# Performance work log

Hardware: AMD Instinct MI355X
Metric: run time of the kernel (lower is better)

The kernel has to match this reference:

```python
import jax, jax.numpy as jnp
import numpy as np

EMBED_DIM = 768
NUM_HEADS = 12
HEAD_DIM = EMBED_DIM // NUM_HEADS


def setup_inputs() -> dict:
    key = jax.random.key(0)
    k1, k2, k3, k4, k5 = jax.random.split(key, 5)
    B, S, D = 2, 4096, EMBED_DIM
    scale = 1.0 / np.sqrt(D)
    return {
        "x": jax.random.normal(k1, (B, S, D), dtype=jnp.float32),
        "Wqkv": jax.random.normal(k2, (D, 3 * D), dtype=jnp.float32) * scale,
        "bqkv": jax.random.normal(k3, (3 * D,), dtype=jnp.float32) * 0.02,
        "Wout": jax.random.normal(k4, (D, D), dtype=jnp.float32) * scale,
        "bout": jax.random.normal(k5, (D,), dtype=jnp.float32) * 0.02,
    }


def reference(x, Wqkv, bqkv, Wout, bout):
    B, S, D = x.shape
    H, Hd = NUM_HEADS, HEAD_DIM
    # fused QKV projection: [B,S,3D]
    qkv = x @ Wqkv + bqkv
    q, k, v = jnp.split(qkv, 3, axis=-1)
    # [B,S,D] -> [B,H,S,Hd]
    q = q.reshape(B, S, H, Hd).transpose(0, 2, 1, 3)
    k = k.reshape(B, S, H, Hd).transpose(0, 2, 1, 3)
    v = v.reshape(B, S, H, Hd).transpose(0, 2, 1, 3)
    # causal SDPA (dropout_p = 0)
    scores = jnp.einsum("bhsd,bhtd->bhst", q, k) / jnp.sqrt(jnp.asarray(Hd, x.dtype))
    causal = jnp.tril(jnp.ones((S, S), dtype=bool))  # [S,S]
    scores = jnp.where(causal[None, None], scores, jnp.finfo(x.dtype).min)
    attn = jax.nn.softmax(scores, axis=-1)
    y = jnp.einsum("bhst,bhtd->bhsd", attn, v)  # [B,H,S,Hd]
    y = y.transpose(0, 2, 1, 3).reshape(B, S, D)
    return y @ Wout + bout
```

## Files before the change

### kernel.cpp

```cpp
#include <hip/hip_runtime.h>

#define S_LEN 4096
#define NH 12
#define HD 64
#define DMODEL 768
#define BATCH 2
#define MTOT (BATCH * S_LEN)

typedef __bf16 bf16x8 __attribute__((ext_vector_type(8)));
typedef __bf16 bf16x4 __attribute__((ext_vector_type(4)));
typedef float f32x4 __attribute__((ext_vector_type(4)));
typedef float f32x8 __attribute__((ext_vector_type(8)));

#define SM_SCALE_LOG2E 0.18033688f
#define SLAB_STRIDE 8448

__device__ __forceinline__ f32x4 f32x4_zero() {
  f32x4 z = {0.f, 0.f, 0.f, 0.f};
  return z;
}

__device__ __forceinline__ void async16(const __bf16* g, void* l) {
  __builtin_amdgcn_global_load_lds(
      (const __attribute__((address_space(1))) void*)g,
      (__attribute__((address_space(3))) void*)l, 16, 0, 0);
}

__global__ __launch_bounds__(256) void cvt_f32_bf16(const float* __restrict__ in,
                                                    __bf16* __restrict__ out, int n8) {
  int i = blockIdx.x * 256 + threadIdx.x;
  if (i >= n8) return;
  f32x8 a = ((const f32x8*)in)[i];
  bf16x8 o;
#pragma unroll
  for (int j = 0; j < 8; ++j) o[j] = (__bf16)a[j];
  ((bf16x8*)out)[i] = o;
}

__global__ __launch_bounds__(256) void transpose_cvt(const float* __restrict__ in,
                                                     __bf16* __restrict__ out, int N) {
  __shared__ __bf16 t[64][72];
  int kb = blockIdx.x * 64, nb = blockIdx.y * 64;
  int c = threadIdx.x & 63, r0 = threadIdx.x >> 6;
#pragma unroll
  for (int i = 0; i < 16; ++i) {
    int r = r0 * 16 + i;
    t[c][r] = (__bf16)in[(size_t)(kb + r) * N + nb + c];
  }
  __syncthreads();
#pragma unroll
  for (int i = 0; i < 16; ++i) {
    int r = r0 * 16 + i;
    out[(size_t)(nb + r) * DMODEL + kb + c] = t[r][c];
  }
}

__device__ __forceinline__ void gemm128_bt(const __bf16* __restrict__ A,
                                           const __bf16* __restrict__ Bt,
                                           int m0, int n0, int K,
                                           __bf16* Alds, __bf16* Blds,
                                           f32x4 acc[4][4]) {
  const int tid = threadIdx.x;
  const int l = tid & 63, w = tid >> 6;
  const int wr = w >> 1, wc = w & 1;
  const int g = l >> 4, ln = l & 15;

  const int rr = tid >> 3;
  const int sx = (tid & 7) ^ (rr & 7);
  const __bf16* As = A + (size_t)(m0 + rr) * K + sx * 8;
  const __bf16* Bs = Bt + (size_t)(n0 + rr) * K + sx * 8;
  char* Ad = (char*)Alds + (w << 10);
  char* Bd = (char*)Blds + (w << 10);

  for (int k0 = 0; k0 < K; k0 += 64) {
#pragma unroll
    for (int i = 0; i < 4; ++i) {
      async16(As + (size_t)(i * 32) * K + k0, Ad + i * 4096);
      async16(Bs + (size_t)(i * 32) * K + k0, Bd + i * 4096);
    }
    __syncthreads();
#pragma unroll
    for (int kk = 0; kk < 2; ++kk) {
      bf16x8 af[4], bfr[4];
#pragma unroll
      for (int mi = 0; mi < 4; ++mi) {
        int row = wr * 64 + mi * 16 + ln;
        af[mi] = *(const bf16x8*)(Alds + row * 64 + ((((kk << 2) + g) ^ (row & 7)) << 3));
      }
#pragma unroll
      for (int ni = 0; ni < 4; ++ni) {
        int row = wc * 64 + ni * 16 + ln;
        bfr[ni] = *(const bf16x8*)(Blds + row * 64 + ((((kk << 2) + g) ^ (row & 7)) << 3));
      }
#pragma unroll
      for (int mi = 0; mi < 4; ++mi)
#pragma unroll
        for (int ni = 0; ni < 4; ++ni)
          acc[mi][ni] =
              __builtin_amdgcn_mfma_f32_16x16x32_bf16(af[mi], bfr[ni], acc[mi][ni], 0, 0, 0);
    }
    __syncthreads();
  }
}

__global__ __launch_bounds__(256) void gemm_qkv(const __bf16* __restrict__ xb,
                                                const __bf16* __restrict__ Wt,
                                                const float* __restrict__ bqkv,
                                                __bf16* __restrict__ Qo,
                                                __bf16* __restrict__ Ko,
                                                __bf16* __restrict__ Vto) {
  __shared__ __bf16 Alds[128 * 64];
  __shared__ __bf16 Blds[128 * 64];
  int bm = blockIdx.x & 63, bn = blockIdx.x >> 6;
  int m0 = bm * 128, n0 = bn * 128;
  f32x4 acc[4][4];
#pragma unroll
  for (int i = 0; i < 4; ++i)
#pragma unroll
    for (int j = 0; j < 4; ++j) acc[i][j] = f32x4_zero();
  gemm128_bt(xb, Wt, m0, n0, DMODEL, Alds, Blds, acc);

  const int l = threadIdx.x & 63, w = threadIdx.x >> 6;
  const int wr = w >> 1, wc = w & 1, g = l >> 4, ln = l & 15;
#pragma unroll
  for (int ni = 0; ni < 4; ++ni) {
    int ncol = n0 + wc * 64 + ni * 16 + ln;
    int which = ncol / DMODEL;
    int dd = ncol - which * DMODEL;
    int h = dd >> 6, hd = dd & 63;
    float bias = bqkv[ncol];
    if (which == 2) {
#pragma unroll
      for (int mi = 0; mi < 4; ++mi)
#pragma unroll
        for (int r = 0; r < 4; ++r) {
          int mrow = m0 + wr * 64 + mi * 16 + 4 * g + r;
          int b = mrow >> 12, s = mrow & (S_LEN - 1);
          float v = acc[mi][ni][r] + bias;
          Vto[(((size_t)(b * NH + h) * HD) + hd) * S_LEN + s] = (__bf16)v;
        }
    } else {
      __bf16* op = (which == 0) ? Qo : Ko;
      const float scl = (which == 0) ? SM_SCALE_LOG2E : 1.0f;
#pragma unroll
      for (int mi = 0; mi < 4; ++mi)
#pragma unroll
        for (int r = 0; r < 4; ++r) {
          int mrow = m0 + wr * 64 + mi * 16 + 4 * g + r;
          int b = mrow >> 12, s = mrow & (S_LEN - 1);
          float v = (acc[mi][ni][r] + bias) * scl;
          op[((((size_t)b * NH + h) * S_LEN) + s) * HD + hd] = (__bf16)v;
        }
    }
  }
}

__global__ __launch_bounds__(256) void gemm_out(const __bf16* __restrict__ yb,
                                                const __bf16* __restrict__ Wt,
                                                const float* __restrict__ bout,
                                                float* __restrict__ out) {
  __shared__ __bf16 Alds[128 * 64];
  __shared__ __bf16 Blds[128 * 64];
  int bm = blockIdx.x & 63, bn = blockIdx.x >> 6;
  int m0 = bm * 128, n0 = bn * 128;
  f32x4 acc[4][4];
#pragma unroll
  for (int i = 0; i < 4; ++i)
#pragma unroll
    for (int j = 0; j < 4; ++j) acc[i][j] = f32x4_zero();
  gemm128_bt(yb, Wt, m0, n0, DMODEL, Alds, Blds, acc);

  const int l = threadIdx.x & 63, w = threadIdx.x >> 6;
  const int wr = w >> 1, wc = w & 1, g = l >> 4, ln = l & 15;
#pragma unroll
  for (int ni = 0; ni < 4; ++ni) {
    int ncol = n0 + wc * 64 + ni * 16 + ln;
    float bias = bout[ncol];
#pragma unroll
    for (int mi = 0; mi < 4; ++mi)
#pragma unroll
      for (int r = 0; r < 4; ++r) {
        int mrow = m0 + wr * 64 + mi * 16 + 4 * g + r;
        out[(size_t)mrow * DMODEL + ncol] = acc[mi][ni][r] + bias;
      }
  }
}

__global__ __launch_bounds__(256) void attn_fwd17(const __bf16* __restrict__ Q,
                                                  const __bf16* __restrict__ K,
                                                  const __bf16* __restrict__ Vt,
                                                  __bf16* __restrict__ Y,
                                                  char* __restrict__ Po) {
  __shared__ __bf16 KVl[2][2][4096];
  __shared__ char Plb[4][2048];

  const int tid = threadIdx.x;
  const int wv = tid >> 6, l = tid & 63;
  const int g = l >> 4, ln = l & 15;
  const int bi = blockIdx.x;
  const int xcd = bi & 7, j = bi >> 3;
  const int head = xcd * 3 + (j % 3);
  const int r_ = j / 3;

  int c, part, np;
  bool split;
  if (r_ < 64) {
    c = 63 - (r_ >> 2);
    part = r_ & 3;
    np = 4;
    split = true;
  } else if (r_ < 112) {
    int q = r_ - 64;
    c = 47 - q / 3;
    part = q % 3;
    np = 3;
    split = true;
  } else if (r_ < 144) {
    int q = r_ - 112;
    c = 31 - (q >> 1);
    part = q & 1;
    np = 2;
    split = true;
  } else {
    c = 159 - r_;
    part = 0;
    np = 1;
    split = false;
  }
  const int T = c + 1;
  const int base = T / np, rem = T % np;
  const int t0 = part * base + (part < rem ? part : rem);
  const int t1 = t0 + base + (part < rem ? 1 : 0);

  const int q0 = 64 * c + 16 * wv;
  const int thr = 16 * wv + ln;
  const bool hasDiag = (t1 == T);

  const size_t hb = (size_t)head * (S_LEN * HD);
  const __bf16* Qh = Q + hb;
  const __bf16* Kh = K + hb;
  const __bf16* Vh = Vt + hb;

  const int sw = (ln & 7) << 4;
  char* Pw = Plb[wv] + ln * 128;

  const int r0 = tid >> 3;
  const int s0 = (tid & 7) ^ (r0 & 7);
  const size_t kL0 = (size_t)r0 * HD + s0 * 8;
  const size_t kL1 = kL0 + (size_t)32 * HD;
  const size_t vL0 = (size_t)r0 * S_LEN + s0 * 8;
  const size_t vL1 = vL0 + (size_t)32 * S_LEN;
  const int ldsoff = wv << 10;

  bf16x8 qf[2];
#pragma unroll
  for (int t = 0; t < 2; ++t)
    qf[t] = *(const bf16x8*)(Qh + (size_t)(q0 + ln) * HD + 32 * t + 8 * g);

  bf16x8 ones;
#pragma unroll
  for (int t = 0; t < 8; ++t) ones[t] = (__bf16)1.0f;

  f32x4 o[4], o5;
#pragma unroll
  for (int nt = 0; nt < 4; ++nt) o[nt] = f32x4_zero();
  o5 = f32x4_zero();

  const __bf16* kq = Kh + (size_t)t0 * 64 * HD;
  const __bf16* vq = Vh + t0 * 64;
  {
    char* Kd = (char*)&KVl[0][0][0] + ldsoff;
    char* Vd = (char*)&KVl[0][1][0] + ldsoff;
    async16(kq + kL0, Kd);
    async16(kq + kL1, Kd + 4096);
    async16(vq + vL0, Vd);
    async16(vq + vL1, Vd + 4096);
    __syncthreads();
  }
  kq += (size_t)64 * HD;
  vq += 64;

  int cur = 0;
  for (int i = t0; i < t1; ++i) {
    const bool more = (i + 1) < t1;
    if (more) {
      char* Kd = (char*)&KVl[cur ^ 1][0][0] + ldsoff;
      char* Vd = (char*)&KVl[cur ^ 1][1][0] + ldsoff;
      async16(kq + kL0, Kd);
      async16(kq + kL1, Kd + 4096);
      async16(vq + vL0, Vd);
      async16(vq + vL1, Vd + 4096);
      kq += (size_t)64 * HD;
      vq += 64;
    }

    const __bf16* Kl = &KVl[cur][0][0];
    const __bf16* Vl = &KVl[cur][1][0];
    const bool diag = hasDiag && (i == c);

    if (!diag) {
#pragma unroll
      for (int jt = 0; jt < 4; ++jt) {
        int row = 16 * jt + ln;
        bf16x8 kf0 = *(const bf16x8*)(Kl + row * 64 + ((g ^ (row & 7)) << 3));
        bf16x8 kf1 = *(const bf16x8*)(Kl + row * 64 + (((4 + g) ^ (row & 7)) << 3));
        f32x4 z = f32x4_zero();
        z = __builtin_amdgcn_mfma_f32_16x16x32_bf16(kf0, qf[0], z, 0, 0, 0);
        z = __builtin_amdgcn_mfma_f32_16x16x32_bf16(kf1, qf[1], z, 0, 0, 0);
        bf16x4 qd;
#pragma unroll
        for (int r = 0; r < 4; ++r) qd[r] = (__bf16)__builtin_exp2f(z[r]);
        *(bf16x4*)(Pw + ((32 * jt + 8 * g) ^ sw)) = qd;
      }
    } else {
#pragma unroll
      for (int jt = 0; jt < 4; ++jt) {
        int row = 16 * jt + ln;
        bf16x8 kf0 = *(const bf16x8*)(Kl + row * 64 + ((g ^ (row & 7)) << 3));
        bf16x8 kf1 = *(const bf16x8*)(Kl + row * 64 + (((4 + g) ^ (row & 7)) << 3));
        f32x4 z = f32x4_zero();
        z = __builtin_amdgcn_mfma_f32_16x16x32_bf16(kf0, qf[0], z, 0, 0, 0);
        z = __builtin_amdgcn_mfma_f32_16x16x32_bf16(kf1, qf[1], z, 0, 0, 0);
        bf16x4 qd;
#pragma unroll
        for (int r = 0; r < 4; ++r) {
          float pv = __builtin_exp2f(z[r]);
          if (16 * jt + 4 * g + r > thr) pv = 0.f;
          qd[r] = (__bf16)pv;
        }
        *(bf16x4*)(Pw + ((32 * jt + 8 * g) ^ sw)) = qd;
      }
    }

    bf16x8 pa0 = *(const bf16x8*)(Pw + ((16 * g) ^ sw));
    bf16x8 pa1 = *(const bf16x8*)(Pw + ((64 + 16 * g) ^ sw));
    __builtin_amdgcn_s_setprio(1);
    o5 = __builtin_amdgcn_mfma_f32_16x16x32_bf16(pa0, ones, o5, 0, 0, 0);
    o5 = __builtin_amdgcn_mfma_f32_16x16x32_bf16(pa1, ones, o5, 0, 0, 0);
#pragma unroll
    for (int nt = 0; nt < 4; ++nt) {
      int row = 16 * nt + ln;
      bf16x8 vf0 = *(const bf16x8*)(Vl + row * 64 + ((g ^ (row & 7)) << 3));
      bf16x8 vf1 = *(const bf16x8*)(Vl + row * 64 + (((4 + g) ^ (row & 7)) << 3));
      o[nt] = __builtin_amdgcn_mfma_f32_16x16x32_bf16(pa0, vf0, o[nt], 0, 0, 0);
      o[nt] = __builtin_amdgcn_mfma_f32_16x16x32_bf16(pa1, vf1, o[nt], 0, 0, 0);
    }
    __builtin_amdgcn_s_setprio(0);

    if (more) __syncthreads();
    cur ^= 1;
  }

  if (!split) {
    const int bb = head / NH, hh = head - bb * NH;
    __bf16* Yp = Y + ((size_t)bb * S_LEN) * DMODEL + hh * HD;
#pragma unroll
    for (int r = 0; r < 4; ++r) {
      float inv = 1.0f / o5[r];
      int qr = q0 + 4 * g + r;
#pragma unroll
      for (int nt = 0; nt < 4; ++nt)
        Yp[(size_t)qr * DMODEL + 16 * nt + ln] = (__bf16)(o[nt][r] * inv);
    }
  } else {
    int soff;
    if (c < 32) soff = (c - 16) * 2 + part;
    else if (c < 48) soff = 32 + (c - 32) * 3 + part;
    else soff = 80 + (c - 48) * 4 + part;
    char* slab = Po + ((size_t)head * 144 + soff) * SLAB_STRIDE;
#pragma unroll
    for (int r = 0; r < 4; ++r) {
      int rowL = 16 * wv + 4 * g + r;
#pragma unroll
      for (int nt = 0; nt < 4; ++nt)
        *(__bf16*)(slab + (rowL * 64 + 16 * nt + ln) * 2) = (__bf16)o[nt][r];
      if (ln == 0) *(float*)(slab + 8192 + rowL * 4) = o5[r];
    }
  }
}

__global__ __launch_bounds__(256) void attn_combine(const char* __restrict__ Po,
                                                    __bf16* __restrict__ Y) {
  const int blk = blockIdx.x;
  const int head = blk / 96, rem = blk - head * 96;
  const int cc = rem >> 1, half = rem & 1;
  const int c = cc + 16;
  int np, boff;
  if (c < 32) {
    np = 2;
    boff = (c - 16) * 2;
  } else if (c < 48) {
    np = 3;
    boff = 32 + (c - 32) * 3;
  } else {
    np = 4;
    boff = 80 + (c - 48) * 4;
  }
  const char* s = Po + ((size_t)head * 144 + boff) * SLAB_STRIDE;
  const int tid = threadIdx.x;
  const int row = half * 32 + (tid >> 3), d0 = (tid & 7) * 8;

  float acc[8] = {0.f, 0.f, 0.f, 0.f, 0.f, 0.f, 0.f, 0.f};
  float rs = 0.f;
  for (int p = 0; p < np; ++p) {
    bf16x8 a = *(const bf16x8*)(s + (size_t)p * SLAB_STRIDE + (row * 64 + d0) * 2);
#pragma unroll
    for (int j = 0; j < 8; ++j) acc[j] += (float)a[j];
    rs += *(const float*)(s + (size_t)p * SLAB_STRIDE + 8192 + row * 4);
  }
  float inv = 1.0f / rs;

  const int bb = head / NH, hh = head - bb * NH;
  __bf16* yp = Y + ((size_t)bb * S_LEN + 64 * c + row) * DMODEL + hh * HD + d0;
  bf16x8 o;
#pragma unroll
  for (int j = 0; j < 8; ++j) o[j] = (__bf16)(acc[j] * inv);
  *(bf16x8*)yp = o;
}

extern "C" void kernel_launch(void* const* d_in, const int* in_sizes, int n_in,
                              void* d_out, int out_size, void* d_ws, size_t ws_size,
                              hipStream_t stream) {
  const float* x = (const float*)d_in[0];
  const float* Wqkv = (const float*)d_in[1];
  const float* bqkv = (const float*)d_in[2];
  const float* Wout = (const float*)d_in[3];
  const float* bout = (const float*)d_in[4];
  float* out = (float*)d_out;

  char* ws = (char*)d_ws;
  size_t off = 0;
  auto take = [&](size_t bytes) {
    char* p = ws + off;
    off += bytes;
    return p;
  };
  const size_t MD2 = (size_t)MTOT * DMODEL * 2;
  __bf16* xb = (__bf16*)take(MD2);
  __bf16* Wqkv_t = (__bf16*)take((size_t)3 * DMODEL * DMODEL * 2);
  __bf16* Wout_t = (__bf16*)take((size_t)DMODEL * DMODEL * 2);
  __bf16* Qb = (__bf16*)take(MD2);
  __bf16* Kb = (__bf16*)take(MD2);
  __bf16* Vtb = (__bf16*)take(MD2);
  __bf16* Yb = (__bf16*)take(MD2);
  char* Po = take((size_t)24 * 144 * SLAB_STRIDE);

  int n8 = MTOT * DMODEL / 8;
  cvt_f32_bf16<<<(n8 + 255) / 256, 256, 0, stream>>>(x, xb, n8);
  transpose_cvt<<<dim3(DMODEL / 64, 3 * DMODEL / 64), 256, 0, stream>>>(Wqkv, Wqkv_t, 3 * DMODEL);
  transpose_cvt<<<dim3(DMODEL / 64, DMODEL / 64), 256, 0, stream>>>(Wout, Wout_t, DMODEL);
  gemm_qkv<<<64 * (3 * DMODEL / 128), 256, 0, stream>>>(xb, Wqkv_t, bqkv, Qb, Kb, Vtb);
  attn_fwd17<<<3840, 256, 0, stream>>>(Qb, Kb, Vtb, Yb, Po);
  attn_combine<<<2304, 256, 0, stream>>>(Po, Yb);
  gemm_out<<<64 * (DMODEL / 128), 256, 0, stream>>>(Yb, Wout_t, bout, out);
}
```

Measured before the change: 179.1 us.

## Double attention query tile to 128 rows with 512-thread blocks

The attention kernel now handles 128 query rows per block with 8 waves instead of 64 rows with 4 waves. Each K/V tile loaded into LDS is reused by twice as many queries, halving K/V global traffic and the number of blocks. The causal-split schedule, partial slab layout and combine indexing are rescaled to match. Waves whose rows lie entirely before a key tile skip its compute but still join the barrier, which adds some idle time on diagonal tiles.

```diff
diff --git a/kernel.cpp b/kernel.cpp
--- a/kernel.cpp
+++ b/kernel.cpp
@@ -13,7 +13,7 @@
 typedef float f32x8 __attribute__((ext_vector_type(8)));
 
 #define SM_SCALE_LOG2E 0.18033688f
-#define SLAB_STRIDE 8448
+#define SLAB_STRIDE 16896
 
 __device__ __forceinline__ f32x4 f32x4_zero() {
   f32x4 z = {0.f, 0.f, 0.f, 0.f};
@@ -186,13 +186,13 @@
   }
 }
 
-__global__ __launch_bounds__(256) void attn_fwd17(const __bf16* __restrict__ Q,
+__global__ __launch_bounds__(512) void attn_fwd18(const __bf16* __restrict__ Q,
                                                   const __bf16* __restrict__ K,
                                                   const __bf16* __restrict__ Vt,
                                                   __bf16* __restrict__ Y,
                                                   char* __restrict__ Po) {
   __shared__ __bf16 KVl[2][2][4096];
-  __shared__ char Plb[4][2048];
+  __shared__ char Plb[8][2048];
 
   const int tid = threadIdx.x;
   const int wv = tid >> 6, l = tid & 63;
@@ -204,37 +204,35 @@
 
   int c, part, np;
   bool split;
-  if (r_ < 64) {
-    c = 63 - (r_ >> 2);
+  if (r_ < 32) {
+    c = 31 - (r_ >> 2);
     part = r_ & 3;
     np = 4;
     split = true;
-  } else if (r_ < 112) {
-    int q = r_ - 64;
-    c = 47 - q / 3;
+  } else if (r_ < 56) {
+    int q = r_ - 32;
+    c = 23 - q / 3;
     part = q % 3;
     np = 3;
     split = true;
-  } else if (r_ < 144) {
-    int q = r_ - 112;
-    c = 31 - (q >> 1);
+  } else if (r_ < 72) {
+    int q = r_ - 56;
+    c = 15 - (q >> 1);
     part = q & 1;
     np = 2;
     split = true;
   } else {
-    c = 159 - r_;
+    c = 79 - r_;
     part = 0;
     np = 1;
     split = false;
   }
-  const int T = c + 1;
+  const int T = 2 * c + 2;
   const int base = T / np, rem = T % np;
   const int t0 = part * base + (part < rem ? part : rem);
   const int t1 = t0 + base + (part < rem ? 1 : 0);
 
-  const int q0 = 64 * c + 16 * wv;
-  const int thr = 16 * wv + ln;
-  const bool hasDiag = (t1 == T);
+  const int q0 = 128 * c + 16 * wv;
 
   const size_t hb = (size_t)head * (S_LEN * HD);
   const __bf16* Qh = Q + hb;
@@ -246,10 +244,8 @@
 
   const int r0 = tid >> 3;
   const int s0 = (tid & 7) ^ (r0 & 7);
-  const size_t kL0 = (size_t)r0 * HD + s0 * 8;
-  const size_t kL1 = kL0 + (size_t)32 * HD;
-  const size_t vL0 = (size_t)r0 * S_LEN + s0 * 8;
-  const size_t vL1 = vL0 + (size_t)32 * S_LEN;
+  const size_t kL = (size_t)r0 * HD + s0 * 8;
+  const size_t vL = (size_t)r0 * S_LEN + s0 * 8;
   const int ldsoff = wv << 10;
 
   bf16x8 qf[2];
@@ -269,12 +265,8 @@
   const __bf16* kq = Kh + (size_t)t0 * 64 * HD;
   const __bf16* vq = Vh + t0 * 64;
   {
-    char* Kd = (char*)&KVl[0][0][0] + ldsoff;
-    char* Vd = (char*)&KVl[0][1][0] + ldsoff;
-    async16(kq + kL0, Kd);
-    async16(kq + kL1, Kd + 4096);
-    async16(vq + vL0, Vd);
-    async16(vq + vL1, Vd + 4096);
+    async16(kq + kL, (char*)&KVl[0][0][0] + ldsoff);
+    async16(vq + vL, (char*)&KVl[0][1][0] + ldsoff);
     __syncthreads();
   }
   kq += (size_t)64 * HD;
@@ -284,68 +276,67 @@
   for (int i = t0; i < t1; ++i) {
     const bool more = (i + 1) < t1;
     if (more) {
-      char* Kd = (char*)&KVl[cur ^ 1][0][0] + ldsoff;
-      char* Vd = (char*)&KVl[cur ^ 1][1][0] + ldsoff;
-      async16(kq + kL0, Kd);
-      async16(kq + kL1, Kd + 4096);
-      async16(vq + vL0, Vd);
-      async16(vq + vL1, Vd + 4096);
+      async16(kq + kL, (char*)&KVl[cur ^ 1][0][0] + ldsoff);
+      async16(vq + vL, (char*)&KVl[cur ^ 1][1][0] + ldsoff);
       kq += (size_t)64 * HD;
       vq += 64;
     }
 
     const __bf16* Kl = &KVl[cur][0][0];
     const __bf16* Vl = &KVl[cur][1][0];
-    const bool diag = hasDiag && (i == c);
-
-    if (!diag) {
-#pragma unroll
-      for (int jt = 0; jt < 4; ++jt) {
-        int row = 16 * jt + ln;
-        bf16x8 kf0 = *(const bf16x8*)(Kl + row * 64 + ((g ^ (row & 7)) << 3));
-        bf16x8 kf1 = *(const bf16x8*)(Kl + row * 64 + (((4 + g) ^ (row & 7)) << 3));
-        f32x4 z = f32x4_zero();
-        z = __builtin_amdgcn_mfma_f32_16x16x32_bf16(kf0, qf[0], z, 0, 0, 0);
-        z = __builtin_amdgcn_mfma_f32_16x16x32_bf16(kf1, qf[1], z, 0, 0, 0);
-        bf16x4 qd;
-#pragma unroll
-        for (int r = 0; r < 4; ++r) qd[r] = (__bf16)__builtin_exp2f(z[r]);
-        *(bf16x4*)(Pw + ((32 * jt + 8 * g) ^ sw)) = qd;
+    const int rel = q0 - 64 * i;
+
+    if (rel > -16) {
+      if (rel >= 63) {
+#pragma unroll
+        for (int jt = 0; jt < 4; ++jt) {
+          int row = 16 * jt + ln;
+          bf16x8 kf0 = *(const bf16x8*)(Kl + row * 64 + ((g ^ (row & 7)) << 3));
+          bf16x8 kf1 = *(const bf16x8*)(Kl + row * 64 + (((4 + g) ^ (row & 7)) << 3));
+          f32x4 z = f32x4_zero();
+          z = __builtin_amdgcn_mfma_f32_16x16x32_bf16(kf0, qf[0], z, 0, 0, 0);
+          z = __builtin_amdgcn_mfma_f32_16x16x32_bf16(kf1, qf[1], z, 0, 0, 0);
+          bf16x4 qd;
+#pragma unroll
+          for (int r = 0; r < 4; ++r) qd[r] = (__bf16)__builtin_exp2f(z[r]);
+          *(bf16x4*)(Pw + ((32 * jt + 8 * g) ^ sw)) = qd;
+        }
+      } else {
+        const int thr = rel + ln;
+#pragma unroll
+        for (int jt = 0; jt < 4; ++jt) {
+          int row = 16 * jt + ln;
+          bf16x8 kf0 = *(const bf16x8*)(Kl + row * 64 + ((g ^ (row & 7)) << 3));
+          bf16x8 kf1 = *(const bf16x8*)(Kl + row * 64 + (((4 + g) ^ (row & 7)) << 3));
+          f32x4 z = f32x4_zero();
+          z = __builtin_amdgcn_mfma_f32_16x16x32_bf16(kf0, qf[0], z, 0, 0, 0);
+          z = __builtin_amdgcn_mfma_f32_16x16x32_bf16(kf1, qf[1], z, 0, 0, 0);
+          bf16x4 qd;
+#pragma unroll
+          for (int r = 0; r < 4; ++r) {
+            float pv = __builtin_exp2f(z[r]);
+            if (16 * jt + 4 * g + r > thr) pv = 0.f;
+            qd[r] = (__bf16)pv;
+          }
+          *(bf16x4*)(Pw + ((32 * jt + 8 * g) ^ sw)) = qd;
+        }
       }
-    } else {
-#pragma unroll
-      for (int jt = 0; jt < 4; ++jt) {
-        int row = 16 * jt + ln;
-        bf16x8 kf0 = *(const bf16x8*)(Kl + row * 64 + ((g ^ (row & 7)) << 3));
-        bf16x8 kf1 = *(const bf16x8*)(Kl + row * 64 + (((4 + g) ^ (row & 7)) << 3));
-        f32x4 z = f32x4_zero();
-        z = __builtin_amdgcn_mfma_f32_16x16x32_bf16(kf0, qf[0], z, 0, 0, 0);
-        z = __builtin_amdgcn_mfma_f32_16x16x32_bf16(kf1, qf[1], z, 0, 0, 0);
-        bf16x4 qd;
-#pragma unroll
-        for (int r = 0; r < 4; ++r) {
-          float pv = __builtin_exp2f(z[r]);
-          if (16 * jt + 4 * g + r > thr) pv = 0.f;
-          qd[r] = (__bf16)pv;
-        }
-        *(bf16x4*)(Pw + ((32 * jt + 8 * g) ^ sw)) = qd;
+
+      bf16x8 pa0 = *(const bf16x8*)(Pw + ((16 * g) ^ sw));
+      bf16x8 pa1 = *(const bf16x8*)(Pw + ((64 + 16 * g) ^ sw));
+      __builtin_amdgcn_s_setprio(1);
+      o5 = __builtin_amdgcn_mfma_f32_16x16x32_bf16(pa0, ones, o5, 0, 0, 0);
+      o5 = __builtin_amdgcn_mfma_f32_16x16x32_bf16(pa1, ones, o5, 0, 0, 0);
+#pragma unroll
+      for (int nt = 0; nt < 4; ++nt) {
+        int row = 16 * nt + ln;
+        bf16x8 vf0 = *(const bf16x8*)(Vl + row * 64 + ((g ^ (row & 7)) << 3));
+        bf16x8 vf1 = *(const bf16x8*)(Vl + row * 64 + (((4 + g) ^ (row & 7)) << 3));
+        o[nt] = __builtin_amdgcn_mfma_f32_16x16x32_bf16(pa0, vf0, o[nt], 0, 0, 0);
+        o[nt] = __builtin_amdgcn_mfma_f32_16x16x32_bf16(pa1, vf1, o[nt], 0, 0, 0);
       }
-    }
-
-    bf16x8 pa0 = *(const bf16x8*)(Pw + ((16 * g) ^ sw));
-    bf16x8 pa1 = *(const bf16x8*)(Pw + ((64 + 16 * g) ^ sw));
-    __builtin_amdgcn_s_setprio(1);
-    o5 = __builtin_amdgcn_mfma_f32_16x16x32_bf16(pa0, ones, o5, 0, 0, 0);
-    o5 = __builtin_amdgcn_mfma_f32_16x16x32_bf16(pa1, ones, o5, 0, 0, 0);
-#pragma unroll
-    for (int nt = 0; nt < 4; ++nt) {
-      int row = 16 * nt + ln;
-      bf16x8 vf0 = *(const bf16x8*)(Vl + row * 64 + ((g ^ (row & 7)) << 3));
-      bf16x8 vf1 = *(const bf16x8*)(Vl + row * 64 + (((4 + g) ^ (row & 7)) << 3));
-      o[nt] = __builtin_amdgcn_mfma_f32_16x16x32_bf16(pa0, vf0, o[nt], 0, 0, 0);
-      o[nt] = __builtin_amdgcn_mfma_f32_16x16x32_bf16(pa1, vf1, o[nt], 0, 0, 0);
-    }
-    __builtin_amdgcn_s_setprio(0);
+      __builtin_amdgcn_s_setprio(0);
+    }
 
     if (more) __syncthreads();
     cur ^= 1;
@@ -364,17 +355,17 @@
     }
   } else {
     int soff;
-    if (c < 32) soff = (c - 16) * 2 + part;
-    else if (c < 48) soff = 32 + (c - 32) * 3 + part;
-    else soff = 80 + (c - 48) * 4 + part;
-    char* slab = Po + ((size_t)head * 144 + soff) * SLAB_STRIDE;
+    if (c < 16) soff = (c - 8) * 2 + part;
+    else if (c < 24) soff = 16 + (c - 16) * 3 + part;
+    else soff = 40 + (c - 24) * 4 + part;
+    char* slab = Po + ((size_t)head * 72 + soff) * SLAB_STRIDE;
 #pragma unroll
     for (int r = 0; r < 4; ++r) {
       int rowL = 16 * wv + 4 * g + r;
 #pragma unroll
       for (int nt = 0; nt < 4; ++nt)
         *(__bf16*)(slab + (rowL * 64 + 16 * nt + ln) * 2) = (__bf16)o[nt][r];
-      if (ln == 0) *(float*)(slab + 8192 + rowL * 4) = o5[r];
+      if (ln == 0) *(float*)(slab + 16384 + rowL * 4) = o5[r];
     }
   }
 }
@@ -383,22 +374,22 @@
                                                     __bf16* __restrict__ Y) {
   const int blk = blockIdx.x;
   const int head = blk / 96, rem = blk - head * 96;
-  const int cc = rem >> 1, half = rem & 1;
-  const int c = cc + 16;
+  const int cc = rem >> 2, quarter = rem & 3;
+  const int c = cc + 8;
   int np, boff;
-  if (c < 32) {
+  if (c < 16) {
     np = 2;
-    boff = (c - 16) * 2;
-  } else if (c < 48) {
+    boff = (c - 8) * 2;
+  } else if (c < 24) {
     np = 3;
-    boff = 32 + (c - 32) * 3;
+    boff = 16 + (c - 16) * 3;
   } else {
     np = 4;
-    boff = 80 + (c - 48) * 4;
-  }
-  const char* s = Po + ((size_t)head * 144 + boff) * SLAB_STRIDE;
+    boff = 40 + (c - 24) * 4;
+  }
+  const char* s = Po + ((size_t)head * 72 + boff) * SLAB_STRIDE;
   const int tid = threadIdx.x;
-  const int row = half * 32 + (tid >> 3), d0 = (tid & 7) * 8;
+  const int row = quarter * 32 + (tid >> 3), d0 = (tid & 7) * 8;
 
   float acc[8] = {0.f, 0.f, 0.f, 0.f, 0.f, 0.f, 0.f, 0.f};
   float rs = 0.f;
@@ -406,12 +397,12 @@
     bf16x8 a = *(const bf16x8*)(s + (size_t)p * SLAB_STRIDE + (row * 64 + d0) * 2);
 #pragma unroll
     for (int j = 0; j < 8; ++j) acc[j] += (float)a[j];
-    rs += *(const float*)(s + (size_t)p * SLAB_STRIDE + 8192 + row * 4);
+    rs += *(const float*)(s + (size_t)p * SLAB_STRIDE + 16384 + row * 4);
   }
   float inv = 1.0f / rs;
 
   const int bb = head / NH, hh = head - bb * NH;
-  __bf16* yp = Y + ((size_t)bb * S_LEN + 64 * c + row) * DMODEL + hh * HD + d0;
+  __bf16* yp = Y + ((size_t)bb * S_LEN + 128 * c + row) * DMODEL + hh * HD + d0;
   bf16x8 o;
 #pragma unroll
   for (int j = 0; j < 8; ++j) o[j] = (__bf16)(acc[j] * inv);
@@ -443,14 +434,14 @@
   __bf16* Kb = (__bf16*)take(MD2);
   __bf16* Vtb = (__bf16*)take(MD2);
   __bf16* Yb = (__bf16*)take(MD2);
-  char* Po = take((size_t)24 * 144 * SLAB_STRIDE);
+  char* Po = take((size_t)24 * 72 * SLAB_STRIDE);
 
   int n8 = MTOT * DMODEL / 8;
   cvt_f32_bf16<<<(n8 + 255) / 256, 256, 0, stream>>>(x, xb, n8);
   transpose_cvt<<<dim3(DMODEL / 64, 3 * DMODEL / 64), 256, 0, stream>>>(Wqkv, Wqkv_t, 3 * DMODEL);
   transpose_cvt<<<dim3(DMODEL / 64, DMODEL / 64), 256, 0, stream>>>(Wout, Wout_t, DMODEL);
   gemm_qkv<<<64 * (3 * DMODEL / 128), 256, 0, stream>>>(xb, Wqkv_t, bqkv, Qb, Kb, Vtb);
-  attn_fwd17<<<3840, 256, 0, stream>>>(Qb, Kb, Vtb, Yb, Po);
+  attn_fwd18<<<1920, 512, 0, stream>>>(Qb, Kb, Vtb, Yb, Po);
   attn_combine<<<2304, 256, 0, stream>>>(Po, Yb);
   gemm_out<<<64 * (DMODEL / 128), 256, 0, stream>>>(Yb, Wout_t, bout, out);
 }
```

Measured after the change: 172.4 us. -3.7%, faster.
